# Performance work log

Hardware: AMD Instinct MI355X
Metric: run time of the kernel (lower is better)

The kernel has to match this reference:

```python
import jax, jax.numpy as jnp
import numpy as np
import math

NUM_GRIDS = 128
INPUT_DIM = 128
OUTPUT_DIM = 128
BATCH = 8192
INIT_SCALE = 0.1


def _borders_cdf_grid(n_chunks):
    # inverse Laplace CDF grid borders, exactly as in the torch module
    def inv(u):
        return np.log(2.0 * u) if u <= 0.5 else -np.log(2.0 * (1.0 - u))
    cs = 1.0 / n_chunks
    b = [inv(i * cs) for i in range(1, n_chunks)]
    left = b[0] - (b[1] - b[0])
    right = b[-1] + (b[-1] - b[-2])
    return np.array([left] + b + [right], dtype=np.float32)  # [n_chunks+1]


def setup_inputs() -> dict:
    key = jax.random.key(0)
    kx, kp = jax.random.split(key)
    x = jax.random.normal(kx, (INPUT_DIM, BATCH), dtype=jnp.float32)
    s = INIT_SCALE / math.sqrt(INPUT_DIM)
    func_parameter = jax.random.uniform(
        kp, (NUM_GRIDS + 1, OUTPUT_DIM, INPUT_DIM), dtype=jnp.float32,
        minval=-s, maxval=s)
    borders = jnp.asarray(_borders_cdf_grid(NUM_GRIDS))
    inverse_chunk_lengths = 1.0 / (borders[1:] - borders[:-1])  # [NUM_GRIDS]
    return {"x": x, "func_parameter": func_parameter,
            "borders": borders, "inverse_chunk_lengths": inverse_chunk_lengths}


def reference(x, func_parameter, borders, inverse_chunk_lengths):
    # x: [I, B]; func_parameter: [G+1, O, I]
    G = borders.shape[0] - 1
    I = x.shape[0]
    # Laplace CDF: R -> [0, 1]
    exp_na = jnp.exp(-jnp.abs(x))
    cdf = jnp.where(x > 0, 1.0 - 0.5 * exp_na, 0.5 * exp_na)
    # bucketize on uniform CDF grid (truncation == floor since cdf*G >= 0)
    idx = jnp.clip((cdf * G).astype(jnp.int32), 0, G - 1)        # [I, B]
    idx_next = jnp.clip(idx + 1, 0, G)                           # [I, B]
    left = borders[idx]                                          # [I, B]
    inv_len = inverse_chunk_lengths[idx]                         # [I, B]
    d = (x - left) * inv_len                                     # [I, B]
    # gather per-input-dim parameter rows: val[i, b, o] = P[idx[i,b], o, i]
    Pt = jnp.transpose(func_parameter, (2, 0, 1))                # [I, G+1, O]
    rows = jnp.arange(I)[:, None]                                # [I, 1]
    val_l = Pt[rows, idx]                                        # [I, B, O]
    val_r = Pt[rows, idx_next]                                   # [I, B, O]
    out = ((1.0 - d)[..., None] * val_l + d[..., None] * val_r).sum(axis=0)  # [B, O]
    return out.T                                                 # [O, B]
```

## Files before the change

### kernel.cpp

```cpp
#include <hip/hip_runtime.h>
#include <cstdint>


#define NG 128
#define NI 128
#define NO 128
#define NB 8192
#define WO 4
#define PH 8
#define NPH (NI / PH)

using half2v = __attribute__((ext_vector_type(2))) _Float16;

__device__ inline uint32_t pack_f16x2(float lo, float hi) {
    _Float16 hl = (_Float16)lo, hh = (_Float16)hi;
    return (uint32_t)__builtin_bit_cast(unsigned short, hl) |
           ((uint32_t)__builtin_bit_cast(unsigned short, hh) << 16);
}

__global__ __launch_bounds__(256) void build_q(const float* __restrict__ P,
                                               uint32_t* __restrict__ Q2) {
    __shared__ float lp[32][129];
    __shared__ float ln[32][129];
    const int g  = blockIdx.x >> 2;
    const int o0 = (blockIdx.x & 3) * 32;
    const int t  = threadIdx.x;
    #pragma unroll
    for (int p = 0; p < 16; ++p) {
        int e = p * 256 + t;
        int ol = e >> 7, i = e & 127;
        lp[ol][i] = P[(size_t)(g * NO + o0 + ol) * NI + i];
        ln[ol][i] = P[(size_t)((g + 1) * NO + o0 + ol) * NI + i];
    }
    __syncthreads();
    #pragma unroll
    for (int p = 0; p < 4; ++p) {
        int e = p * 256 + t;
        int sl = e >> 7, i = e & 127;
        uint32_t r[4];
        #pragma unroll
        for (int ow = 0; ow < 4; ++ow) {
            float pl = lp[sl * 4 + ow][i];
            float dd = ln[sl * 4 + ow][i] - pl;
            r[ow] = pack_f16x2(pl, dd);
        }
        int s = (o0 >> 2) + sl;
        *(uint4*)(Q2 + ((size_t)(s * NI + i) * NG + g) * 4) =
            make_uint4(r[0], r[1], r[2], r[3]);
    }
}

__global__ __launch_bounds__(256) void build_t(const float* __restrict__ x,
                                               const float* __restrict__ borders,
                                               const float* __restrict__ icl,
                                               uint32_t* __restrict__ T) {
    const int e0 = (blockIdx.x * 256 + threadIdx.x) * 4;
    const float4 xv = *(const float4*)(x + e0);
    uint32_t r[4];
    const float xs[4] = {xv.x, xv.y, xv.z, xv.w};
    #pragma unroll
    for (int k = 0; k < 4; ++k) {
        float v = xs[k];
        float ea = __expf(-fabsf(v));
        float cdf = v > 0.f ? 1.f - 0.5f * ea : 0.5f * ea;
        int idx = (int)(cdf * 128.f);
        idx = idx > 127 ? 127 : idx;
        float d = (v - borders[idx]) * icl[idx];
        _Float16 hd = (_Float16)d;
        r[k] = ((uint32_t)idx << 4) |
               ((uint32_t)__builtin_bit_cast(unsigned short, hd) << 16);
    }
    *(uint4*)(T + e0) = make_uint4(r[0], r[1], r[2], r[3]);
}

__global__ __launch_bounds__(1024) void main_k(const uint32_t* __restrict__ Q2,
                                               const uint32_t* __restrict__ T,
                                               float* __restrict__ out) {
    __shared__ uint32_t slab[2][PH][NG * WO];
    const int t    = threadIdx.x;
    const int bx   = blockIdx.x;
    const int s    = bx & 31;
    const int bblk = (bx >> 5) << 10;
    const int bme  = bblk + t;
    const uint32_t* Qs = Q2 + (size_t)s * NI * NG * WO;

    float a0 = 0.f, a1 = 0.f, a2 = 0.f, a3 = 0.f;

    uint32_t treg[PH];
    {
        uint4 q0 = *(const uint4*)(Qs + (size_t)t * 4);
        #pragma unroll
        for (int il = 0; il < PH; ++il)
            treg[il] = T[(size_t)il * NB + bme];
        ((uint4*)&slab[0][0][0])[t] = q0;
    }
    __syncthreads();

    #pragma unroll
    for (int p = 0; p < NPH; ++p) {
        const int cur = p & 1;
        uint32_t tnxt[PH];
        uint4 qnxt;
        if (p < NPH - 1) {
            qnxt = *(const uint4*)(Qs + (size_t)(p + 1) * (PH * NG * WO) +
                                   (size_t)t * 4);
            #pragma unroll
            for (int il = 0; il < PH; ++il)
                tnxt[il] = T[(size_t)((p + 1) * PH + il) * NB + bme];
        }
        #pragma unroll
        for (int il = 0; il < PH; ++il) {
            uint32_t tw  = treg[il];
            uint32_t off = tw & 0xFFFFu;
            uint32_t w2b = (tw & 0xFFFF0000u) | 0x3C00u;
            uint4 q = *(const uint4*)((const char*)&slab[cur][il][0] + off);
            half2v w2 = __builtin_bit_cast(half2v, w2b);
            a0 = __builtin_amdgcn_fdot2(__builtin_bit_cast(half2v, q.x), w2, a0, false);
            a1 = __builtin_amdgcn_fdot2(__builtin_bit_cast(half2v, q.y), w2, a1, false);
            a2 = __builtin_amdgcn_fdot2(__builtin_bit_cast(half2v, q.z), w2, a2, false);
            a3 = __builtin_amdgcn_fdot2(__builtin_bit_cast(half2v, q.w), w2, a3, false);
        }
        if (p < NPH - 1) {
            ((uint4*)&slab[cur ^ 1][0][0])[t] = qnxt;
            #pragma unroll
            for (int il = 0; il < PH; ++il)
                treg[il] = tnxt[il];
            __syncthreads();
        }
    }

    size_t ob = (size_t)(s * 4) * NB + bme;
    __builtin_nontemporal_store(a0, out + ob);
    __builtin_nontemporal_store(a1, out + ob + NB);
    __builtin_nontemporal_store(a2, out + ob + 2 * (size_t)NB);
    __builtin_nontemporal_store(a3, out + ob + 3 * (size_t)NB);
}

extern "C" void kernel_launch(void* const* d_in, const int* in_sizes, int n_in,
                              void* d_out, int out_size, void* d_ws, size_t ws_size,
                              hipStream_t stream) {
    const float* x       = (const float*)d_in[0];
    const float* P       = (const float*)d_in[1];
    const float* borders = (const float*)d_in[2];
    const float* icl     = (const float*)d_in[3];
    float* out = (float*)d_out;

    uint32_t* Q2 = (uint32_t*)d_ws;
    uint32_t* T  = Q2 + (size_t)NO * NI * NG;

    hipLaunchKernelGGL(build_q, dim3(NG * 4), dim3(256), 0, stream, P, Q2);
    hipLaunchKernelGGL(build_t, dim3(NI * NB / 1024), dim3(256), 0, stream,
                       x, borders, icl, T);
    hipLaunchKernelGGL(main_k, dim3((NB / 1024) * 32), dim3(1024), 0, stream,
                       Q2, T, out);
}
```

Measured before the change: 94.97 us.

## Split input dim across blocks with 32-output slabs, async LDS loads and reduction

Reorganizes the main kernel so each block handles 16 input dims, 32 outputs and 1024 batch rows, with each thread computing 8 batch rows by 4 outputs. Parameter slabs are streamed into LDS with global_load_lds. Partial sums for 8 input chunks are written to a workspace and summed by a new reduce kernel that also transposes to [O,B]. The goal is more work per thread and cheaper staging, in exchange for about 32MB of extra partial traffic and one more kernel launch.

```diff
diff --git a/kernel.cpp b/kernel.cpp
--- a/kernel.cpp
+++ b/kernel.cpp
@@ -6,9 +6,6 @@
 #define NI 128
 #define NO 128
 #define NB 8192
-#define WO 4
-#define PH 8
-#define NPH (NI / PH)
 
 using half2v = __attribute__((ext_vector_type(2))) _Float16;
 
@@ -18,12 +15,19 @@
            ((uint32_t)__builtin_bit_cast(unsigned short, hh) << 16);
 }
 
+__device__ inline void load_lds16(const uint32_t* g, uint32_t* l) {
+    __builtin_amdgcn_global_load_lds(
+        (const __attribute__((address_space(1))) uint32_t*)g,
+        (__attribute__((address_space(3))) uint32_t*)l, 16, 0, 0);
+}
+
 __global__ __launch_bounds__(256) void build_q(const float* __restrict__ P,
-                                               uint32_t* __restrict__ Q2) {
+                                               uint32_t* __restrict__ Q3) {
     __shared__ float lp[32][129];
     __shared__ float ln[32][129];
     const int g  = blockIdx.x >> 2;
-    const int o0 = (blockIdx.x & 3) * 32;
+    const int os = blockIdx.x & 3;
+    const int o0 = os * 32;
     const int t  = threadIdx.x;
     #pragma unroll
     for (int p = 0; p < 16; ++p) {
@@ -33,21 +37,21 @@
         ln[ol][i] = P[(size_t)((g + 1) * NO + o0 + ol) * NI + i];
     }
     __syncthreads();
+    const int i   = t >> 1;
+    const int om0 = (t & 1) * 16;
+    uint32_t r[16];
     #pragma unroll
-    for (int p = 0; p < 4; ++p) {
-        int e = p * 256 + t;
-        int sl = e >> 7, i = e & 127;
-        uint32_t r[4];
-        #pragma unroll
-        for (int ow = 0; ow < 4; ++ow) {
-            float pl = lp[sl * 4 + ow][i];
-            float dd = ln[sl * 4 + ow][i] - pl;
-            r[ow] = pack_f16x2(pl, dd);
-        }
-        int s = (o0 >> 2) + sl;
-        *(uint4*)(Q2 + ((size_t)(s * NI + i) * NG + g) * 4) =
-            make_uint4(r[0], r[1], r[2], r[3]);
+    for (int j = 0; j < 16; ++j) {
+        int om = om0 + j;
+        float pl = lp[om][i];
+        float dd = ln[om][i] - pl;
+        r[j] = pack_f16x2(pl, dd);
     }
+    uint32_t* dst = Q3 + ((size_t)(os * NI + i) * NG + g) * 32 + om0;
+    *(uint4*)(dst)      = make_uint4(r[0],  r[1],  r[2],  r[3]);
+    *(uint4*)(dst + 4)  = make_uint4(r[4],  r[5],  r[6],  r[7]);
+    *(uint4*)(dst + 8)  = make_uint4(r[8],  r[9],  r[10], r[11]);
+    *(uint4*)(dst + 12) = make_uint4(r[12], r[13], r[14], r[15]);
 }
 
 __global__ __launch_bounds__(256) void build_t(const float* __restrict__ x,
@@ -67,73 +71,105 @@
         idx = idx > 127 ? 127 : idx;
         float d = (v - borders[idx]) * icl[idx];
         _Float16 hd = (_Float16)d;
-        r[k] = ((uint32_t)idx << 4) |
+        r[k] = ((uint32_t)idx << 7) |
                ((uint32_t)__builtin_bit_cast(unsigned short, hd) << 16);
     }
     *(uint4*)(T + e0) = make_uint4(r[0], r[1], r[2], r[3]);
 }
 
-__global__ __launch_bounds__(1024) void main_k(const uint32_t* __restrict__ Q2,
+__global__ __launch_bounds__(1024) void main_k(const uint32_t* __restrict__ Q3,
                                                const uint32_t* __restrict__ T,
-                                               float* __restrict__ out) {
-    __shared__ uint32_t slab[2][PH][NG * WO];
-    const int t    = threadIdx.x;
-    const int bx   = blockIdx.x;
-    const int s    = bx & 31;
-    const int bblk = (bx >> 5) << 10;
-    const int bme  = bblk + t;
-    const uint32_t* Qs = Q2 + (size_t)s * NI * NG * WO;
+                                               float* __restrict__ part) {
+    __shared__ uint32_t slab[2][4096];
+    const int t   = threadIdx.x;
+    const int bx  = blockIdx.x;
+    const int wid = ((bx & 7) << 5) | (bx >> 3);
+    const int bt  = wid & 7;
+    const int os  = (wid >> 3) & 3;
+    const int ic  = wid >> 5;
+    const int w = t >> 6, l = t & 63;
+    const int q = l & 7;
+    const int bbase = (bt << 10) + (w << 6) + ((l >> 3) << 3);
+    const uint32_t qoff = (uint32_t)q << 4;
+    const uint32_t* Qs = Q3 + ((size_t)os * NI + ic * 16) * (NG * 32) + t * 4;
+    const uint32_t* Ts = T + (size_t)(ic * 16) * NB + bbase;
 
-    float a0 = 0.f, a1 = 0.f, a2 = 0.f, a3 = 0.f;
+    float4 acc[8];
+    #pragma unroll
+    for (int r = 0; r < 8; ++r) acc[r] = make_float4(0.f, 0.f, 0.f, 0.f);
 
-    uint32_t treg[PH];
-    {
-        uint4 q0 = *(const uint4*)(Qs + (size_t)t * 4);
-        #pragma unroll
-        for (int il = 0; il < PH; ++il)
-            treg[il] = T[(size_t)il * NB + bme];
-        ((uint4*)&slab[0][0][0])[t] = q0;
-    }
+    load_lds16(Qs, &slab[0][t * 4]);
+    uint4 ta = *(const uint4*)(Ts);
+    uint4 tb = *(const uint4*)(Ts + 4);
     __syncthreads();
 
     #pragma unroll
-    for (int p = 0; p < NPH; ++p) {
-        const int cur = p & 1;
-        uint32_t tnxt[PH];
-        uint4 qnxt;
-        if (p < NPH - 1) {
-            qnxt = *(const uint4*)(Qs + (size_t)(p + 1) * (PH * NG * WO) +
-                                   (size_t)t * 4);
-            #pragma unroll
-            for (int il = 0; il < PH; ++il)
-                tnxt[il] = T[(size_t)((p + 1) * PH + il) * NB + bme];
+    for (int ii = 0; ii < 16; ++ii) {
+        const int cur = ii & 1;
+        if (ii < 15) {
+            load_lds16(Qs + (ii + 1) * (NG * 32), &slab[cur ^ 1][t * 4]);
         }
+        uint4 na, nb;
+        if (ii < 15) {
+            na = *(const uint4*)(Ts + (size_t)(ii + 1) * NB);
+            nb = *(const uint4*)(Ts + (size_t)(ii + 1) * NB + 4);
+        }
+        const char* sp = (const char*)&slab[cur][0];
+        const uint32_t tc[8] = {ta.x, ta.y, ta.z, ta.w, tb.x, tb.y, tb.z, tb.w};
         #pragma unroll
-        for (int il = 0; il < PH; ++il) {
-            uint32_t tw  = treg[il];
-            uint32_t off = tw & 0xFFFFu;
+        for (int r = 0; r < 8; ++r) {
+            uint32_t tw  = tc[r];
+            uint32_t off = (tw & 0xFFFFu) | qoff;
             uint32_t w2b = (tw & 0xFFFF0000u) | 0x3C00u;
-            uint4 q = *(const uint4*)((const char*)&slab[cur][il][0] + off);
+            uint4 qv = *(const uint4*)(sp + off);
             half2v w2 = __builtin_bit_cast(half2v, w2b);
-            a0 = __builtin_amdgcn_fdot2(__builtin_bit_cast(half2v, q.x), w2, a0, false);
-            a1 = __builtin_amdgcn_fdot2(__builtin_bit_cast(half2v, q.y), w2, a1, false);
-            a2 = __builtin_amdgcn_fdot2(__builtin_bit_cast(half2v, q.z), w2, a2, false);
-            a3 = __builtin_amdgcn_fdot2(__builtin_bit_cast(half2v, q.w), w2, a3, false);
+            acc[r].x = __builtin_amdgcn_fdot2(__builtin_bit_cast(half2v, qv.x), w2, acc[r].x, false);
+            acc[r].y = __builtin_amdgcn_fdot2(__builtin_bit_cast(half2v, qv.y), w2, acc[r].y, false);
+            acc[r].z = __builtin_amdgcn_fdot2(__builtin_bit_cast(half2v, qv.z), w2, acc[r].z, false);
+            acc[r].w = __builtin_amdgcn_fdot2(__builtin_bit_cast(half2v, qv.w), w2, acc[r].w, false);
         }
-        if (p < NPH - 1) {
-            ((uint4*)&slab[cur ^ 1][0][0])[t] = qnxt;
-            #pragma unroll
-            for (int il = 0; il < PH; ++il)
-                treg[il] = tnxt[il];
+        if (ii < 15) {
+            ta = na; tb = nb;
             __syncthreads();
         }
     }
 
-    size_t ob = (size_t)(s * 4) * NB + bme;
-    __builtin_nontemporal_store(a0, out + ob);
-    __builtin_nontemporal_store(a1, out + ob + NB);
-    __builtin_nontemporal_store(a2, out + ob + 2 * (size_t)NB);
-    __builtin_nontemporal_store(a3, out + ob + 3 * (size_t)NB);
+    float* pp = part + ((size_t)ic * NB + bbase) * NO + os * 32 + (q << 2);
+    #pragma unroll
+    for (int r = 0; r < 8; ++r)
+        *(float4*)(pp + (size_t)r * NO) = acc[r];
+}
+
+__global__ __launch_bounds__(256) void reduce_k(const float* __restrict__ part,
+                                                float* __restrict__ out) {
+    __shared__ float ts[NO][17];
+    const int t  = threadIdx.x;
+    const int b0 = blockIdx.x * 16;
+    #pragma unroll
+    for (int p = 0; p < 2; ++p) {
+        const int c  = p * 256 + t;
+        const int bl = c >> 5;
+        const int o4 = (c & 31) * 4;
+        const float* src = part + ((size_t)(b0 + bl)) * NO + o4;
+        float4 s = *(const float4*)(src);
+        #pragma unroll
+        for (int icc = 1; icc < 8; ++icc) {
+            float4 v = *(const float4*)(src + (size_t)icc * NB * NO);
+            s.x += v.x; s.y += v.y; s.z += v.z; s.w += v.w;
+        }
+        ts[o4 + 0][bl] = s.x;
+        ts[o4 + 1][bl] = s.y;
+        ts[o4 + 2][bl] = s.z;
+        ts[o4 + 3][bl] = s.w;
+    }
+    __syncthreads();
+    const int bl  = t & 15;
+    const int orr = t >> 4;
+    #pragma unroll
+    for (int k = 0; k < 8; ++k) {
+        const int o = orr + k * 16;
+        __builtin_nontemporal_store(ts[o][bl], out + (size_t)o * NB + b0 + bl);
+    }
 }
 
 extern "C" void kernel_launch(void* const* d_in, const int* in_sizes, int n_in,
@@ -145,12 +181,13 @@
     const float* icl     = (const float*)d_in[3];
     float* out = (float*)d_out;
 
-    uint32_t* Q2 = (uint32_t*)d_ws;
-    uint32_t* T  = Q2 + (size_t)NO * NI * NG;
+    uint32_t* Q3  = (uint32_t*)d_ws;
+    uint32_t* T   = Q3 + (size_t)4 * NI * NG * 32;
+    float*    prt = (float*)(T + (size_t)NI * NB);
 
-    hipLaunchKernelGGL(build_q, dim3(NG * 4), dim3(256), 0, stream, P, Q2);
+    hipLaunchKernelGGL(build_q, dim3(NG * 4), dim3(256), 0, stream, P, Q3);
     hipLaunchKernelGGL(build_t, dim3(NI * NB / 1024), dim3(256), 0, stream,
                        x, borders, icl, T);
-    hipLaunchKernelGGL(main_k, dim3((NB / 1024) * 32), dim3(1024), 0, stream,
-                       Q2, T, out);
+    hipLaunchKernelGGL(main_k, dim3(256), dim3(1024), 0, stream, Q3, T, prt);
+    hipLaunchKernelGGL(reduce_k, dim3(NB / 16), dim3(256), 0, stream, prt, out);
 }
```

Result: slower. 310.2 us (+226.6%).

## Split input dimension across two blocks with partial-sum reduce; widen build_q tiles

Applied to the files above, without the earlier changes.

The main kernel now splits the 128 input dimensions into two halves, doubling the grid to 512 blocks so more CUs are occupied. Each half writes a partial output buffer, and a new reduce kernel adds the two. build_q is retiled so each block handles 4 grid points and 16 outputs, loading 5 grid slabs once instead of reloading neighbours. This adds an extra kernel launch and a full 2×O×B partial write and read, in exchange for better GPU occupancy (256 blocks of 1024 threads previously).

```diff
diff --git a/kernel.cpp b/kernel.cpp
--- a/kernel.cpp
+++ b/kernel.cpp
@@ -8,9 +8,9 @@
 #define NB 8192
 #define WO 4
 #define PH 8
-#define NPH (NI / PH)
 
 using half2v = __attribute__((ext_vector_type(2))) _Float16;
+using float4v = __attribute__((ext_vector_type(4))) float;
 
 __device__ inline uint32_t pack_f16x2(float lo, float hi) {
     _Float16 hl = (_Float16)lo, hh = (_Float16)hi;
@@ -20,33 +20,38 @@
 
 __global__ __launch_bounds__(256) void build_q(const float* __restrict__ P,
                                                uint32_t* __restrict__ Q2) {
-    __shared__ float lp[32][129];
-    __shared__ float ln[32][129];
-    const int g  = blockIdx.x >> 2;
-    const int o0 = (blockIdx.x & 3) * 32;
+    __shared__ float L[5][16][128];
+    const int gb = blockIdx.x >> 3;
+    const int ob = blockIdx.x & 7;
+    const int g0 = gb * 4;
+    const int o0 = ob * 16;
+    const int s0 = ob * 4;
     const int t  = threadIdx.x;
     #pragma unroll
-    for (int p = 0; p < 16; ++p) {
-        int e = p * 256 + t;
-        int ol = e >> 7, i = e & 127;
-        lp[ol][i] = P[(size_t)(g * NO + o0 + ol) * NI + i];
-        ln[ol][i] = P[(size_t)((g + 1) * NO + o0 + ol) * NI + i];
+    for (int pass = 0; pass < 40; ++pass) {
+        int row = pass * 2 + (t >> 7);
+        int i   = t & 127;
+        int gg  = row >> 4, ol = row & 15;
+        L[gg][ol][i] = P[(size_t)(g0 + gg) * (NO * NI) + (o0 + ol) * NI + i];
     }
     __syncthreads();
     #pragma unroll
-    for (int p = 0; p < 4; ++p) {
-        int e = p * 256 + t;
-        int sl = e >> 7, i = e & 127;
-        uint32_t r[4];
+    for (int pp = 0; pp < 2; ++pp) {
+        int item = pp * 256 + t;
+        int i  = item & 127;
+        int sl = item >> 7;
+        uint32_t* dst = Q2 + ((size_t)((s0 + sl) * NI + i) * NG + g0) * 4;
         #pragma unroll
-        for (int ow = 0; ow < 4; ++ow) {
-            float pl = lp[sl * 4 + ow][i];
-            float dd = ln[sl * 4 + ow][i] - pl;
-            r[ow] = pack_f16x2(pl, dd);
+        for (int gg = 0; gg < 4; ++gg) {
+            uint32_t r[4];
+            #pragma unroll
+            for (int ow = 0; ow < 4; ++ow) {
+                float pl = L[gg][sl * 4 + ow][i];
+                float dd = L[gg + 1][sl * 4 + ow][i] - pl;
+                r[ow] = pack_f16x2(pl, dd);
+            }
+            *(uint4*)(dst + gg * 4) = make_uint4(r[0], r[1], r[2], r[3]);
         }
-        int s = (o0 >> 2) + sl;
-        *(uint4*)(Q2 + ((size_t)(s * NI + i) * NG + g) * 4) =
-            make_uint4(r[0], r[1], r[2], r[3]);
     }
 }
 
@@ -73,16 +78,18 @@
     *(uint4*)(T + e0) = make_uint4(r[0], r[1], r[2], r[3]);
 }
 
-__global__ __launch_bounds__(1024) void main_k(const uint32_t* __restrict__ Q2,
-                                               const uint32_t* __restrict__ T,
-                                               float* __restrict__ out) {
+__global__ __launch_bounds__(1024, 8) void main_k(const uint32_t* __restrict__ Q2,
+                                                  const uint32_t* __restrict__ T,
+                                                  float* __restrict__ part) {
     __shared__ uint32_t slab[2][PH][NG * WO];
     const int t    = threadIdx.x;
     const int bx   = blockIdx.x;
     const int s    = bx & 31;
-    const int bblk = (bx >> 5) << 10;
+    const int ih   = (bx >> 5) & 1;
+    const int bblk = (bx >> 6) << 10;
     const int bme  = bblk + t;
-    const uint32_t* Qs = Q2 + (size_t)s * NI * NG * WO;
+    const uint32_t* Qs = Q2 + ((size_t)s * NI + ih * 64) * (NG * WO);
+    const uint32_t* Ts = T + (size_t)(ih * 64) * NB;
 
     float a0 = 0.f, a1 = 0.f, a2 = 0.f, a3 = 0.f;
 
@@ -91,22 +98,22 @@
         uint4 q0 = *(const uint4*)(Qs + (size_t)t * 4);
         #pragma unroll
         for (int il = 0; il < PH; ++il)
-            treg[il] = T[(size_t)il * NB + bme];
+            treg[il] = Ts[(size_t)il * NB + bme];
         ((uint4*)&slab[0][0][0])[t] = q0;
     }
     __syncthreads();
 
     #pragma unroll
-    for (int p = 0; p < NPH; ++p) {
+    for (int p = 0; p < 8; ++p) {
         const int cur = p & 1;
         uint32_t tnxt[PH];
         uint4 qnxt;
-        if (p < NPH - 1) {
+        if (p < 7) {
             qnxt = *(const uint4*)(Qs + (size_t)(p + 1) * (PH * NG * WO) +
                                    (size_t)t * 4);
             #pragma unroll
             for (int il = 0; il < PH; ++il)
-                tnxt[il] = T[(size_t)((p + 1) * PH + il) * NB + bme];
+                tnxt[il] = Ts[(size_t)((p + 1) * PH + il) * NB + bme];
         }
         #pragma unroll
         for (int il = 0; il < PH; ++il) {
@@ -120,7 +127,7 @@
             a2 = __builtin_amdgcn_fdot2(__builtin_bit_cast(half2v, q.z), w2, a2, false);
             a3 = __builtin_amdgcn_fdot2(__builtin_bit_cast(half2v, q.w), w2, a3, false);
         }
-        if (p < NPH - 1) {
+        if (p < 7) {
             ((uint4*)&slab[cur ^ 1][0][0])[t] = qnxt;
             #pragma unroll
             for (int il = 0; il < PH; ++il)
@@ -129,11 +136,20 @@
         }
     }
 
-    size_t ob = (size_t)(s * 4) * NB + bme;
-    __builtin_nontemporal_store(a0, out + ob);
-    __builtin_nontemporal_store(a1, out + ob + NB);
-    __builtin_nontemporal_store(a2, out + ob + 2 * (size_t)NB);
-    __builtin_nontemporal_store(a3, out + ob + 3 * (size_t)NB);
+    float* po = part + (size_t)ih * (NO * NB) + (size_t)(s * 4) * NB + bme;
+    __builtin_nontemporal_store(a0, po);
+    __builtin_nontemporal_store(a1, po + NB);
+    __builtin_nontemporal_store(a2, po + 2 * (size_t)NB);
+    __builtin_nontemporal_store(a3, po + 3 * (size_t)NB);
+}
+
+__global__ __launch_bounds__(256) void reduce_k(const float* __restrict__ part,
+                                                float* __restrict__ out) {
+    const int e0 = (blockIdx.x * 256 + threadIdx.x) * 4;
+    const float4v v0 = *(const float4v*)(part + e0);
+    const float4v v1 = *(const float4v*)(part + (size_t)NO * NB + e0);
+    const float4v r = v0 + v1;
+    __builtin_nontemporal_store(r, (float4v*)(out + e0));
 }
 
 extern "C" void kernel_launch(void* const* d_in, const int* in_sizes, int n_in,
@@ -147,10 +163,12 @@
 
     uint32_t* Q2 = (uint32_t*)d_ws;
     uint32_t* T  = Q2 + (size_t)NO * NI * NG;
+    float*    prt = (float*)(T + (size_t)NI * NB);
 
-    hipLaunchKernelGGL(build_q, dim3(NG * 4), dim3(256), 0, stream, P, Q2);
+    hipLaunchKernelGGL(build_q, dim3(256), dim3(256), 0, stream, P, Q2);
     hipLaunchKernelGGL(build_t, dim3(NI * NB / 1024), dim3(256), 0, stream,
                        x, borders, icl, T);
-    hipLaunchKernelGGL(main_k, dim3((NB / 1024) * 32), dim3(1024), 0, stream,
-                       Q2, T, out);
+    hipLaunchKernelGGL(main_k, dim3(512), dim3(1024), 0, stream, Q2, T, prt);
+    hipLaunchKernelGGL(reduce_k, dim3(NO * NB / 1024), dim3(256), 0, stream,
+                       prt, out);
 }
```

Result: faster. 92.58 us (-2.5%).
